# Kernel optimization log

Hardware: AMD Instinct MI355X
Metric: run time of the kernel (lower is better)

The kernel has to match this reference:

```python
import jax, jax.numpy as jnp
import numpy as np

_GELU = lambda x: jax.nn.gelu(x, approximate=False)  # torch nn.GELU default = exact erf


def setup_inputs():
    key = jax.random.key(0)
    ks = jax.random.split(key, 32)
    B, H = 16384, 768
    def p(i, shape):
        return jax.random.normal(ks[i], shape, jnp.float32) * 0.02
    return {
        "image_feat": jax.random.normal(ks[0], (B, H), jnp.float32),
        "text_feat": jax.random.normal(ks[1], (B, H), jnp.float32),
        "enhanced_image_feat": jax.random.normal(ks[2], (B, H), jnp.float32),
        "enhanced_text_feat": jax.random.normal(ks[3], (B, H), jnp.float32),
        "missing_type": jax.random.randint(ks[4], (B,), 0, 4),
        # info_encoder: H->256->64
        "info_w1": p(5, (H, 256)), "info_b1": jnp.zeros((256,), jnp.float32),
        "info_w2": p(6, (256, 64)), "info_b2": jnp.zeros((64,), jnp.float32),
        # modality_importance_predictor: H->H/2->1 (dropout inactive at eval)
        "imp_w1": p(7, (H, H // 2)), "imp_b1": jnp.zeros((H // 2,), jnp.float32),
        "imp_w2": p(8, (H // 2, 1)), "imp_b2": jnp.zeros((1,), jnp.float32),
        # feature_discriminator: H->256->64->1
        "disc_w1": p(9, (H, 256)), "disc_b1": jnp.zeros((256,), jnp.float32),
        "disc_w2": p(10, (256, 64)), "disc_b2": jnp.zeros((64,), jnp.float32),
        "disc_w3": p(11, (64, 1)), "disc_b3": jnp.zeros((1,), jnp.float32),
        # consistency_predictor: 2H->H->H/2->1
        "cons_w1": p(12, (2 * H, H)), "cons_b1": jnp.zeros((H,), jnp.float32),
        "cons_w2": p(13, (H, H // 2)), "cons_b2": jnp.zeros((H // 2,), jnp.float32),
        "cons_w3": p(14, (H // 2, 1)), "cons_b3": jnp.zeros((1,), jnp.float32),
        # task_difficulty_predictor: 2H->H->H/2->1
        "diff_w1": p(15, (2 * H, H)), "diff_b1": jnp.zeros((H,), jnp.float32),
        "diff_w2": p(16, (H, H // 2)), "diff_b2": jnp.zeros((H // 2,), jnp.float32),
        "diff_w3": p(17, (H // 2, 1)), "diff_b3": jnp.zeros((1,), jnp.float32),
    }


def _forward(image_feat, text_feat, enhanced_image_feat, enhanced_text_feat,
             info_w1, info_b1, info_w2, info_b2,
             imp_w1, imp_b1, imp_w2, imp_b2,
             disc_w1, disc_b1, disc_w2, disc_b2, disc_w3, disc_b3,
             cons_w1, cons_b1, cons_w2, cons_b2, cons_w3, cons_b3,
             diff_w1, diff_b1, diff_w2, diff_b2, diff_w3, diff_b3):
    sig = jax.nn.sigmoid

    def geometric(f):  # vectorized version of the per-sample python loop
        n = jnp.linalg.norm(f, axis=-1)
        nq = sig((n - 1.0) * 2.0)
        sp = jnp.mean((jnp.abs(f) > 0.01).astype(jnp.float32), axis=-1)
        sq = sig(jnp.std(f, axis=-1, ddof=1) * 10.0 - 1.0)  # torch.std is unbiased
        return (nq + sp + sq) / 3.0

    def information(f):
        enc = _GELU(f @ info_w1 + info_b1) @ info_w2 + info_b2  # [B,64]
        disc = jnp.round(sig(enc) * 10.0).astype(jnp.int32)     # values in 0..10
        # histogram-based entropy == the torch.unique loop (prob = count/64)
        counts = jnp.sum(disc[:, :, None] == jnp.arange(11, dtype=jnp.int32)[None, None, :], axis=1)
        prob = counts.astype(jnp.float32) / enc.shape[-1]
        ent = -jnp.sum(jnp.where(prob > 0, prob * jnp.log(prob + 1e-8), 0.0), axis=-1)
        eq = sig(ent - 2.0)
        # svd of a 1xD matrix has a single singular value = ||f||_2
        n = jnp.linalg.norm(f, axis=-1)
        cq = (n > 0.01).astype(jnp.float32) / f.shape[-1]
        fn = f / jnp.maximum(n, 1e-12)[:, None]  # F.normalize
        dq = sig(jnp.sum(fn * fn, axis=-1) - 0.5)
        return (eq + cq + dq) / 3.0

    def importance(f):
        return sig(_GELU(f @ imp_w1 + imp_b1) @ imp_w2 + imp_b2)[:, 0]

    def discrim(f):
        h = _GELU(f @ disc_w1 + disc_b1)
        h = _GELU(h @ disc_w2 + disc_b2)
        return sig(h @ disc_w3 + disc_b3)[:, 0]

    def head3(f, w1, b1, w2, b2, w3, b3):
        h = _GELU(f @ w1 + b1)
        h = _GELU(h @ w2 + b2)
        return sig(h @ w3 + b3)[:, 0]

    g_img = geometric(image_feat)
    g_txt = geometric(text_feat)
    g_eimg = geometric(enhanced_image_feat)
    g_etxt = geometric(enhanced_text_feat)
    i_img = information(image_feat)
    i_txt = information(text_feat)
    cons_o = head3(jnp.concatenate([image_feat, text_feat], -1), cons_w1, cons_b1, cons_w2, cons_b2, cons_w3, cons_b3)
    cons_e = head3(jnp.concatenate([enhanced_image_feat, enhanced_text_feat], -1), cons_w1, cons_b1, cons_w2, cons_b2, cons_w3, cons_b3)
    imp_i = importance(image_feat)
    imp_t = importance(text_feat)
    imp_ei = importance(enhanced_image_feat)
    imp_et = importance(enhanced_text_feat)
    auth_io = discrim(image_feat)
    auth_ie = discrim(enhanced_image_feat)
    auth_to = discrim(text_feat)
    auth_te = discrim(enhanced_text_feat)
    diff = head3(jnp.concatenate([enhanced_image_feat, enhanced_text_feat], -1), diff_w1, diff_b1, diff_w2, diff_b2, diff_w3, diff_b3)
    overall = (g_img + g_txt + i_img + i_txt + cons_e + (imp_i + imp_t) / 2.0) / 6.0
    return jnp.stack([g_img, g_txt, g_eimg, g_etxt, i_img, i_txt, cons_o, cons_e,
                      imp_i, imp_t, imp_ei, imp_et, auth_io, auth_ie, auth_to, auth_te,
                      diff, overall])  # [18, B]


def reference(image_feat, text_feat, enhanced_image_feat, enhanced_text_feat, missing_type,
              info_w1, info_b1, info_w2, info_b2,
              imp_w1, imp_b1, imp_w2, imp_b2,
              disc_w1, disc_b1, disc_w2, disc_b2, disc_w3, disc_b3,
              cons_w1, cons_b1, cons_w2, cons_b2, cons_w3, cons_b3,
              diff_w1, diff_b1, diff_w2, diff_b2, diff_w3, diff_b3):
    # missing_type is carried by the original forward but never used in the math
    return _forward(image_feat, text_feat, enhanced_image_feat, enhanced_text_feat,
                    info_w1, info_b1, info_w2, info_b2,
                    imp_w1, imp_b1, imp_w2, imp_b2,
                    disc_w1, disc_b1, disc_w2, disc_b2, disc_w3, disc_b3,
                    cons_w1, cons_b1, cons_w2, cons_b2, cons_w3, cons_b3,
                    diff_w1, diff_b1, diff_w2, diff_b2, diff_w3, diff_b3)
```

## Files before the change

kernel.cpp:

```cpp
#include <hip/hip_runtime.h>

typedef unsigned short bfu;
typedef __attribute__((ext_vector_type(8))) __bf16 bf16x8;
typedef __attribute__((ext_vector_type(4))) float f32x4;

__device__ __forceinline__ float bf2f(bfu u) {
    unsigned int x = ((unsigned int)u) << 16;
    return __builtin_bit_cast(float, x);
}
__device__ __forceinline__ bfu f2bf(float f) {
    unsigned int u = __builtin_bit_cast(unsigned int, f);
    unsigned int r = (u + 0x7fffu + ((u >> 16) & 1u)) >> 16;
    return (bfu)r;
}
__device__ __forceinline__ float sigm(float x) { return 1.0f / (1.0f + __expf(-x)); }
__device__ __forceinline__ float gelu_f(float x) {
    const float y = 0.7978845608f * (x + 0.044715f * x * x * x);
    const float t = 1.f - 2.f / (__expf(2.f * y) + 1.f);
    return 0.5f * x * (1.f + t);
}
__device__ __forceinline__ float gelu_x(float x) {
    return 0.5f * x * (1.0f + erff(x * 0.70710678118654752f));
}

__device__ __forceinline__ void async16(const void* g, void* l) {
    __builtin_amdgcn_global_load_lds((const __attribute__((address_space(1))) void*)g,
                                     (__attribute__((address_space(3))) void*)l, 16, 0, 0);
}

struct TDesc { const float* src; bfu* dst; int K, N, blk0; };
struct TPack { TDesc d[9]; };

__global__ __launch_bounds__(256) void transpose_k(TPack p) {
    const int bid = blockIdx.x;
    int j = 0;
#pragma unroll
    for (int i = 1; i < 9; ++i)
        if (bid >= p.d[i].blk0) j = i;
    const TDesc d = p.d[j];
    const int local = bid - d.blk0;
    const int tkn = d.K >> 6;
    const int tk = local % tkn, tn = local / tkn;
    const int k0 = tk * 64, n0 = tn * 64;
    __shared__ float tile[64][65];
    const int tx = threadIdx.x & 63, ty = threadIdx.x >> 6;
#pragma unroll
    for (int i = 0; i < 16; ++i) {
        const int r = ty * 16 + i;
        tile[r][tx] = d.src[(size_t)(k0 + r) * d.N + n0 + tx];
    }
    __syncthreads();
#pragma unroll
    for (int i = 0; i < 16; ++i) {
        const int n = ty * 16 + i;
        d.dst[(size_t)(n0 + n) * d.K + k0 + tx] = f2bf(tile[tx][n]);
    }
}

__global__ __launch_bounds__(256)
void prep_k(float* accz, int nacc, bfu* disc2pad, const float* w3,
            const float* b2, float* w3pad, float* b2pad) {
    const int i = blockIdx.x * 256 + threadIdx.x;
    if (i < nacc) accz[i] = 0.f;
    if (i < 64 * 256) disc2pad[64 * 256 + i] = 0;
    if (i < 128) {
        w3pad[i] = (i < 64) ? w3[i] : 0.f;
        b2pad[i] = (i < 64) ? b2[i] : 0.f;
    }
}

__global__ __launch_bounds__(256)
void geomcast_k(const float* F0, const float* F1, bfu* D0, bfu* D1,
                float* g0, float* g1, float* p0, float* p1) {
    const int z = blockIdx.y;
    const float* F = z ? F1 : F0;
    bfu* D = z ? D1 : D0;
    float* gout = z ? g1 : g0;
    float* part = z ? p1 : p0;
    const int wave = threadIdx.x >> 6, lane = threadIdx.x & 63;
    const int row = blockIdx.x * 4 + wave;
    const float* fr = F + (size_t)row * 768;
    bfu* dr = D + (size_t)row * 768;
    float sum = 0.f, ss = 0.f, cnt = 0.f;
#pragma unroll
    for (int i = 0; i < 3; ++i) {
        const float4 v = *(const float4*)(fr + i * 256 + lane * 4);
        sum += v.x + v.y + v.z + v.w;
        ss += v.x * v.x + v.y * v.y + v.z * v.z + v.w * v.w;
        cnt += ((fabsf(v.x) > 0.01f) ? 1.f : 0.f) + ((fabsf(v.y) > 0.01f) ? 1.f : 0.f) +
               ((fabsf(v.z) > 0.01f) ? 1.f : 0.f) + ((fabsf(v.w) > 0.01f) ? 1.f : 0.f);
        ushort4 b;
        b.x = f2bf(v.x); b.y = f2bf(v.y); b.z = f2bf(v.z); b.w = f2bf(v.w);
        *(ushort4*)(dr + i * 256 + lane * 4) = b;
    }
#pragma unroll
    for (int off = 32; off; off >>= 1) {
        sum += __shfl_xor(sum, off);
        ss  += __shfl_xor(ss, off);
        cnt += __shfl_xor(cnt, off);
    }
    if (lane == 0) {
        const float n = sqrtf(ss);
        const float nq = sigm((n - 1.f) * 2.f);
        const float sp = cnt * (1.f / 768.f);
        float var = (ss - sum * sum * (1.f / 768.f)) * (1.f / 767.f);
        var = fmaxf(var, 0.f);
        const float sq = sigm(sqrtf(var) * 10.f - 1.f);
        gout[row] = (nq + sp + sq) * (1.f / 3.f);
        if (part) {
            const float cq = (n > 0.01f) ? (1.f / 768.f) : 0.f;
            const float nc = fmaxf(n, 1e-12f);
            const float dq = sigm(ss / (nc * nc) - 0.5f);
            part[row] = (cq + dq) * (1.f / 3.f);
        }
    }
}

struct Half {
    const bfu* W;
    const float* bias;
    const float* dotw;
    bfu* C;
    float* acc;
    int ldc, mode;
};
struct Seg {
    const bfu* A; const bfu* A2;
    Half h[2];
    int K, Ksplit, lda, Mtiles;
};
struct SegPack { Seg s[7]; };

__global__ __launch_bounds__(512, 2)
void gemm_k(SegPack p) {
    constexpr int BK = 64;
    __shared__ bfu LDS[65536];
    bfu* As0 = LDS;
    bfu* As1 = LDS + 16384;
    bfu* Ws0 = LDS + 32768;
    bfu* Ws1 = LDS + 49152;

    const int NTt = gridDim.x;
    const int g = blockIdx.y * NTt + blockIdx.x;
    const int G8 = NTt * 8;
    const int m = (g / G8) * 8 + (g & 7);
    const int n = (g % G8) >> 3;
    const Seg sg = p.s[n];
    if (m >= sg.Mtiles) return;
    const int t = threadIdx.x;
    const int wave = t >> 6, lane = t & 63;
    const int row_l = lane & 15, kq = lane >> 4;
    const int m0 = m * 256;
    const int wm = wave >> 2;
    const int wn = wave & 3;
    const int half = wn >> 1;

    const int r0 = t >> 3;
    const int cc = ((t & 7) ^ (r0 & 7)) << 3;
    const bfu* pA[4];
    const bfu* pW[4];
#pragma unroll
    for (int i = 0; i < 4; ++i)
        pA[i] = sg.A + (size_t)(m0 + r0 + 64 * i) * sg.lda + cc;
#pragma unroll
    for (int i = 0; i < 2; ++i) {
        pW[i]     = sg.h[0].W + (size_t)(r0 + 64 * i) * sg.K + cc;
        pW[2 + i] = sg.h[1].W + (size_t)(r0 + 64 * i) * sg.K + cc;
    }
    const int nkt = sg.K >> 6;
    const int ktsw = (sg.Ksplit < sg.K) ? (sg.Ksplit >> 6) : 0x7fffffff;

    f32x4 acc[8][4] = {};

    auto stageA = [&](int sn, bfu* Ad) {
        if (sn == ktsw) {
#pragma unroll
            for (int i = 0; i < 4; ++i)
                pA[i] = sg.A2 + (size_t)(m0 + r0 + 64 * i) * sg.lda + cc;
        }
#pragma unroll
        for (int i = 0; i < 4; ++i)
            async16(pA[i], Ad + ((i * 512 + wave * 64) << 3));
#pragma unroll
        for (int i = 0; i < 4; ++i) pA[i] += BK;
    };
    auto ldF = [&](const bfu* base, int row, int ks) -> bf16x8 {
        return *(const bf16x8*)(base + row * BK + (((ks * 4 + kq) ^ (row & 7)) << 3));
    };

#pragma unroll
    for (int i = 0; i < 4; ++i)
        async16(pW[i], Ws0 + ((i * 512 + wave * 64) << 3));
#pragma unroll
    for (int i = 0; i < 4; ++i) pW[i] += BK;
    stageA(0, As0);
#pragma unroll
    for (int i = 0; i < 4; ++i)
        async16(pW[i], Ws1 + ((i * 512 + wave * 64) << 3));
#pragma unroll
    for (int i = 0; i < 4; ++i) pW[i] += BK;
    asm volatile("s_waitcnt vmcnt(4)" ::: "memory");
    __builtin_amdgcn_s_barrier();

    auto do_iter = [&](bfu* Acur, bfu* Aoth, bfu* Wcur, int kt) {
        bf16x8 af[4], b0[4], b1[4];
#pragma unroll
        for (int q = 0; q < 4; ++q)
            af[q] = ldF(Acur, wm * 128 + q * 16 + row_l, 0);
#pragma unroll
        for (int ni = 0; ni < 4; ++ni) {
            const int rB = wn * 64 + ni * 16 + row_l;
            b0[ni] = ldF(Wcur, rB, 0);
            b1[ni] = ldF(Wcur, rB, 1);
        }
        if (kt + 1 < nkt) stageA(kt + 1, Aoth);
        __builtin_amdgcn_s_barrier();
        asm volatile("s_waitcnt lgkmcnt(0)" ::: "memory");
        __builtin_amdgcn_sched_barrier(0);
        __builtin_amdgcn_s_setprio(1);
#pragma unroll
        for (int q = 0; q < 4; ++q)
#pragma unroll
            for (int ni = 0; ni < 4; ++ni)
                acc[q][ni] = __builtin_amdgcn_mfma_f32_16x16x32_bf16(af[q], b0[ni], acc[q][ni], 0, 0, 0);
        __builtin_amdgcn_s_setprio(0);
        __builtin_amdgcn_s_barrier();
#pragma unroll
        for (int q = 0; q < 4; ++q)
            af[q] = ldF(Acur, wm * 128 + q * 16 + row_l, 1);
        if (kt + 2 < nkt) {
            async16(pW[0], Wcur + ((0 * 512 + wave * 64) << 3));
            async16(pW[1], Wcur + ((1 * 512 + wave * 64) << 3));
        }
        __builtin_amdgcn_s_barrier();
        asm volatile("s_waitcnt lgkmcnt(0)" ::: "memory");
        __builtin_amdgcn_sched_barrier(0);
        __builtin_amdgcn_s_setprio(1);
#pragma unroll
        for (int q = 0; q < 4; ++q)
#pragma unroll
            for (int ni = 0; ni < 4; ++ni)
                acc[q][ni] = __builtin_amdgcn_mfma_f32_16x16x32_bf16(af[q], b1[ni], acc[q][ni], 0, 0, 0);
        __builtin_amdgcn_s_setprio(0);
        __builtin_amdgcn_s_barrier();
#pragma unroll
        for (int q = 0; q < 4; ++q)
            af[q] = ldF(Acur, wm * 128 + 64 + q * 16 + row_l, 0);
        if (kt + 2 < nkt) {
            async16(pW[2], Wcur + ((2 * 512 + wave * 64) << 3));
            async16(pW[3], Wcur + ((3 * 512 + wave * 64) << 3));
#pragma unroll
            for (int i = 0; i < 4; ++i) pW[i] += BK;
        }
        __builtin_amdgcn_s_barrier();
        asm volatile("s_waitcnt lgkmcnt(0)" ::: "memory");
        __builtin_amdgcn_sched_barrier(0);
        __builtin_amdgcn_s_setprio(1);
#pragma unroll
        for (int q = 0; q < 4; ++q)
#pragma unroll
            for (int ni = 0; ni < 4; ++ni)
                acc[4 + q][ni] = __builtin_amdgcn_mfma_f32_16x16x32_bf16(af[q], b0[ni], acc[4 + q][ni], 0, 0, 0);
        __builtin_amdgcn_s_setprio(0);
        __builtin_amdgcn_s_barrier();
#pragma unroll
        for (int q = 0; q < 4; ++q)
            af[q] = ldF(Acur, wm * 128 + 64 + q * 16 + row_l, 1);
        if (kt + 2 < nkt) { asm volatile("s_waitcnt vmcnt(4)" ::: "memory"); }
        else              { asm volatile("s_waitcnt vmcnt(0)" ::: "memory"); }
        __builtin_amdgcn_s_barrier();
        asm volatile("s_waitcnt lgkmcnt(0)" ::: "memory");
        __builtin_amdgcn_sched_barrier(0);
        __builtin_amdgcn_s_setprio(1);
#pragma unroll
        for (int q = 0; q < 4; ++q)
#pragma unroll
            for (int ni = 0; ni < 4; ++ni)
                acc[4 + q][ni] = __builtin_amdgcn_mfma_f32_16x16x32_bf16(af[q], b1[ni], acc[4 + q][ni], 0, 0, 0);
        __builtin_amdgcn_s_setprio(0);
        __builtin_amdgcn_s_barrier();
    };

    for (int kt = 0; kt < nkt; kt += 2) {
        do_iter(As0, As1, Ws0, kt);
        do_iter(As1, As0, Ws1, kt + 1);
    }

    const Half hh = sg.h[half];
    if (hh.mode == 0) {
#pragma unroll
        for (int ni = 0; ni < 4; ++ni) {
            const int lcol = (wn & 1) * 64 + ni * 16 + row_l;
            const float bv = hh.bias[lcol];
#pragma unroll
            for (int mi = 0; mi < 8; ++mi)
#pragma unroll
                for (int r = 0; r < 4; ++r) {
                    const int row = m0 + wm * 128 + mi * 16 + kq * 4 + r;
                    hh.C[(size_t)row * hh.ldc + lcol] = f2bf(gelu_f(acc[mi][ni][r] + bv));
                }
        }
    } else if (hh.mode == 2) {
#pragma unroll
        for (int ni = 0; ni < 4; ++ni) {
            const int lcol = (wn & 1) * 64 + ni * 16 + row_l;
            const float bv = hh.bias[lcol];
#pragma unroll
            for (int mi = 0; mi < 8; ++mi)
#pragma unroll
                for (int r = 0; r < 4; ++r) {
                    const int row = m0 + wm * 128 + mi * 16 + kq * 4 + r;
                    hh.C[(size_t)row * hh.ldc + lcol] = f2bf(gelu_x(acc[mi][ni][r] + bv));
                }
        }
    } else if (hh.mode == 1) {
#pragma unroll
        for (int mi = 0; mi < 8; ++mi)
#pragma unroll
            for (int r = 0; r < 4; ++r) {
                float s = 0.f;
#pragma unroll
                for (int ni = 0; ni < 4; ++ni) {
                    const int lcol = (wn & 1) * 64 + ni * 16 + row_l;
                    s += hh.dotw[lcol] * gelu_f(acc[mi][ni][r] + hh.bias[lcol]);
                }
                s += __shfl_xor(s, 1); s += __shfl_xor(s, 2);
                s += __shfl_xor(s, 4); s += __shfl_xor(s, 8);
                if (row_l == 0)
                    atomicAdd(hh.acc + m0 + wm * 128 + mi * 16 + kq * 4 + r, s);
            }
    }
}

__global__ __launch_bounds__(256)
void gemm64ent_k(const bfu* __restrict__ A, const bfu* __restrict__ W,
                 const float* __restrict__ bias, const float* __restrict__ part,
                 float* out, int B, int K, int lda) {
    constexpr int BK = 64, MT = 2, NT = 4;
    __shared__ __align__(16) float smemf[12288];
    bfu* As0 = (bfu*)smemf;
    bfu* Ws0 = (bfu*)smemf + 128 * BK;
    bfu* As1 = (bfu*)smemf + 192 * BK;
    bfu* Ws1 = (bfu*)smemf + 320 * BK;
    float* ET = smemf;
    const int t = threadIdx.x;
    const int wave = t >> 6, lane = t & 63;
    const int row_l = lane & 15, kq = lane >> 4;
    const int m0 = blockIdx.x * 128;
    const int wrow0 = wave * 32;
    f32x4 acc[MT][NT] = {};
    const int nkt = K / BK;

    const int r0 = t >> 3;
    const int cc = ((t & 7) ^ (r0 & 7)) << 3;
    const size_t strA = (size_t)32 * lda;
    const size_t strW = (size_t)32 * K;
    const bfu* pA[4];
    const bfu* pW[2];
#pragma unroll
    for (int i = 0; i < 4; ++i)
        pA[i] = A + (size_t)(m0 + r0) * lda + cc + i * strA;
#pragma unroll
    for (int i = 0; i < 2; ++i)
        pW[i] = W + (size_t)r0 * K + cc + i * strW;

    auto stage = [&](bfu* Ad, bfu* Wd) {
#pragma unroll
        for (int i = 0; i < 4; ++i)
            async16(pA[i], Ad + ((i * 256 + wave * 64) << 3));
#pragma unroll
        for (int i = 0; i < 2; ++i)
            async16(pW[i], Wd + ((i * 256 + wave * 64) << 3));
#pragma unroll
        for (int i = 0; i < 4; ++i) pA[i] += BK;
#pragma unroll
        for (int i = 0; i < 2; ++i) pW[i] += BK;
    };
    auto compute = [&](const bfu* Ab, const bfu* Wb) {
#pragma unroll
        for (int ks = 0; ks < 2; ++ks) {
            bf16x8 af[MT], bfr[NT];
#pragma unroll
            for (int mi = 0; mi < MT; ++mi) {
                const int rA = wrow0 + mi * 16 + row_l;
                af[mi] = *(const bf16x8*)(Ab + rA * BK + (((ks * 4 + kq) ^ (rA & 7)) << 3));
            }
#pragma unroll
            for (int ni = 0; ni < NT; ++ni) {
                const int rB = ni * 16 + row_l;
                bfr[ni] = *(const bf16x8*)(Wb + rB * BK + (((ks * 4 + kq) ^ (rB & 7)) << 3));
            }
#pragma unroll
            for (int mi = 0; mi < MT; ++mi)
#pragma unroll
                for (int ni = 0; ni < NT; ++ni)
                    acc[mi][ni] = __builtin_amdgcn_mfma_f32_16x16x32_bf16(af[mi], bfr[ni], acc[mi][ni], 0, 0, 0);
        }
    };

    stage(As0, Ws0);
    __syncthreads();
    for (int kt = 0; kt < nkt; kt += 2) {
        stage(As1, Ws1);
        compute(As0, Ws0);
        __syncthreads();
        if (kt + 2 < nkt) stage(As0, Ws0);
        compute(As1, Ws1);
        __syncthreads();
    }

#pragma unroll
    for (int mi = 0; mi < MT; ++mi)
#pragma unroll
        for (int ni = 0; ni < NT; ++ni) {
            const int col = ni * 16 + row_l;
            const float bv = bias[col];
#pragma unroll
            for (int r = 0; r < 4; ++r)
                ET[(wrow0 + mi * 16 + kq * 4 + r) * 65 + col] = acc[mi][ni][r] + bv;
        }
    __syncthreads();
    if (t < 128) {
        int cnt[11];
#pragma unroll
        for (int b = 0; b < 11; ++b) cnt[b] = 0;
        for (int j = 0; j < 64; ++j) {
            const int d = (int)rintf(sigm(ET[t * 65 + j]) * 10.f);
#pragma unroll
            for (int b = 0; b < 11; ++b) cnt[b] += (d == b);
        }
        float ent = 0.f;
#pragma unroll
        for (int b = 0; b < 11; ++b) {
            if (cnt[b] > 0) {
                const float pp = (float)cnt[b] * (1.f / 64.f);
                ent -= pp * __logf(pp + 1e-8f);
            }
        }
        const int row = m0 + t;
        const int orow = (row < B) ? 4 : 5;
        const int rl = (row < B) ? row : row - B;
        out[(size_t)orow * B + rl] = part[row] + sigm(ent - 2.f) * (1.f / 3.f);
    }
}

__global__ __launch_bounds__(256)
void finalize_k(float* out, const float* a_imp1, const float* a_imp2,
                const float* a_co, const float* a_ce, const float* a_df,
                const float* a_d1, const float* a_d2,
                const float* imp_b2, const float* disc_b3,
                const float* cons_b3, const float* diff_b3, int B) {
    const int i = blockIdx.x * 256 + threadIdx.x;
    if (i >= B) return;
    const float ib = imp_b2[0], db = disc_b3[0], cb = cons_b3[0], fb = diff_b3[0];
    const float o6 = sigm(a_co[i] + cb);
    const float o7 = sigm(a_ce[i] + cb);
    const float o8 = sigm(a_imp1[i] + ib);
    const float o9 = sigm(a_imp1[B + i] + ib);
    out[6 * B + i] = o6;
    out[7 * B + i] = o7;
    out[8 * B + i] = o8;
    out[9 * B + i] = o9;
    out[10 * B + i] = sigm(a_imp2[i] + ib);
    out[11 * B + i] = sigm(a_imp2[B + i] + ib);
    out[12 * B + i] = sigm(a_d1[i] + db);
    out[14 * B + i] = sigm(a_d1[B + i] + db);
    out[13 * B + i] = sigm(a_d2[i] + db);
    out[15 * B + i] = sigm(a_d2[B + i] + db);
    out[16 * B + i] = sigm(a_df[i] + fb);
    const float v = out[0 * B + i] + out[1 * B + i] + out[4 * B + i] + out[5 * B + i] +
                    o7 + 0.5f * (o8 + o9);
    out[17 * B + i] = v * (1.f / 6.f);
}

extern "C" void kernel_launch(void* const* d_in, const int* in_sizes, int n_in,
                              void* d_out, int out_size, void* d_ws, size_t ws_size,
                              hipStream_t stream) {
    const int B = in_sizes[4];
    const int B2 = 2 * B;
    float* out = (float*)d_out;
    const float* img  = (const float*)d_in[0];
    const float* txt  = (const float*)d_in[1];
    const float* eimg = (const float*)d_in[2];
    const float* etxt = (const float*)d_in[3];
    const float* info_w1 = (const float*)d_in[5];  const float* info_b1 = (const float*)d_in[6];
    const float* info_w2 = (const float*)d_in[7];  const float* info_b2 = (const float*)d_in[8];
    const float* imp_w1  = (const float*)d_in[9];  const float* imp_b1  = (const float*)d_in[10];
    const float* imp_w2  = (const float*)d_in[11]; const float* imp_b2  = (const float*)d_in[12];
    const float* disc_w1 = (const float*)d_in[13]; const float* disc_b1 = (const float*)d_in[14];
    const float* disc_w2 = (const float*)d_in[15]; const float* disc_b2 = (const float*)d_in[16];
    const float* disc_w3 = (const float*)d_in[17]; const float* disc_b3 = (const float*)d_in[18];
    const float* cons_w1 = (const float*)d_in[19]; const float* cons_b1 = (const float*)d_in[20];
    const float* cons_w2 = (const float*)d_in[21]; const float* cons_b2 = (const float*)d_in[22];
    const float* cons_w3 = (const float*)d_in[23]; const float* cons_b3 = (const float*)d_in[24];
    const float* diff_w1 = (const float*)d_in[25]; const float* diff_b1 = (const float*)d_in[26];
    const float* diff_w2 = (const float*)d_in[27]; const float* diff_b2 = (const float*)d_in[28];
    const float* diff_w3 = (const float*)d_in[29]; const float* diff_b3 = (const float*)d_in[30];

    char* wsp = (char*)d_ws;
    size_t off = 0;
    auto alloc = [&](size_t bytes) -> void* {
        void* p = wsp + off;
        off += (bytes + 255) & ~(size_t)255;
        return p;
    };
    bfu* info1t = (bfu*)alloc((size_t)256 * 768 * 2);
    bfu* info2t = (bfu*)alloc((size_t)64 * 256 * 2);
    bfu* imp1t  = (bfu*)alloc((size_t)384 * 768 * 2);
    bfu* disc1t = (bfu*)alloc((size_t)256 * 768 * 2);
    bfu* disc2p = (bfu*)alloc((size_t)128 * 256 * 2);
    bfu* cons1t = (bfu*)alloc((size_t)768 * 1536 * 2);
    bfu* cons2t = (bfu*)alloc((size_t)384 * 768 * 2);
    bfu* diff1t = (bfu*)alloc((size_t)768 * 1536 * 2);
    bfu* diff2t = (bfu*)alloc((size_t)384 * 768 * 2);
    float* w3pad = (float*)alloc(128 * 4);
    float* b2pad = (float*)alloc(128 * 4);
    float* part = (float*)alloc((size_t)B2 * 4);
    float* accz = (float*)alloc((size_t)11 * B * 4);
    float* a_imp1 = accz;
    float* a_imp2 = accz + B2;
    float* a_co = accz + 2 * B2;
    float* a_ce = a_co + B;
    float* a_df = a_ce + B;
    float* a_d1 = a_df + B;
    float* a_d2 = a_d1 + B2;
    bfu* fA01 = (bfu*)alloc((size_t)B2 * 768 * 2);
    bfu* X    = (bfu*)alloc((size_t)B * 2048 * 2);
    bfu* Hd   = X;
    bfu* Hi   = X + (size_t)B * 512;
    bfu* Hc_c = X + (size_t)B * 512;
    bfu* Hc_d = X + (size_t)B * 1280;
    (void)ws_size; (void)n_in; (void)out_size;

    prep_k<<<dim3((11 * B + 255) / 256), 256, 0, stream>>>(accz, 11 * B, disc2p,
                                                           disc_w3, disc_b2, w3pad, b2pad);
    TPack tp;
    int blk = 0, ti = 0;
    auto setd = [&](const float* s, bfu* d, int K, int N) {
        tp.d[ti++] = {s, d, K, N, blk};
        blk += (K / 64) * (N / 64);
    };
    setd(info_w1, info1t, 768, 256);
    setd(info_w2, info2t, 256, 64);
    setd(imp_w1, imp1t, 768, 384);
    setd(disc_w1, disc1t, 768, 256);
    setd(disc_w2, disc2p, 256, 64);
    setd(cons_w1, cons1t, 1536, 768);
    setd(cons_w2, cons2t, 768, 384);
    setd(diff_w1, diff1t, 1536, 768);
    setd(diff_w2, diff2t, 768, 384);
    transpose_k<<<dim3(blk), 256, 0, stream>>>(tp);

    auto h_st = [&](const bfu* W, const float* b, bfu* C, int ldc, int mode) -> Half {
        return Half{W, b, nullptr, C, nullptr, ldc, mode};
    };
    auto h_dt = [&](const bfu* W, const float* b, const float* dw, float* acc) -> Half {
        return Half{W, b, dw, nullptr, acc, 0, 1};
    };
    auto h_skip = [&](const bfu* W) -> Half {
        return Half{W, nullptr, nullptr, nullptr, nullptr, 0, 3};
    };
    auto seg = [&](const bfu* A, const bfu* A2, Half h0, Half h1,
                   int K, int Ksplit, int lda, int Mt) -> Seg {
        return Seg{A, A2, {h0, h1}, K, Ksplit, lda, Mt};
    };
    const bfu* fB = fA01 + (size_t)B * 768;
    const int MT2 = B2 / 256, MT1 = B / 256;

    geomcast_k<<<dim3(B / 4, 2), 256, 0, stream>>>(img, txt, fA01, (bfu*)fB,
                                                   out + 0 * B, out + 1 * B, part, part + B);
    {
        SegPack p;
        p.s[0] = seg(fA01, nullptr,
                     h_st(info1t, info_b1, Hi, 256, 2),
                     h_st(info1t + (size_t)128 * 768, info_b1 + 128, Hi + 128, 256, 2),
                     768, 768, 768, MT2);
        p.s[1] = seg(fA01, nullptr,
                     h_st(disc1t, disc_b1, Hd, 256, 0),
                     h_st(disc1t + (size_t)128 * 768, disc_b1 + 128, Hd + 128, 256, 0),
                     768, 768, 768, MT2);
        p.s[2] = seg(fA01, nullptr,
                     h_dt(imp1t, imp_b1, imp_w2, a_imp1),
                     h_dt(imp1t + (size_t)128 * 768, imp_b1 + 128, imp_w2 + 128, a_imp1),
                     768, 768, 768, MT2);
        p.s[3] = seg(fA01, nullptr,
                     h_dt(imp1t + (size_t)256 * 768, imp_b1 + 256, imp_w2 + 256, a_imp1),
                     h_skip(imp1t),
                     768, 768, 768, MT2);
        gemm_k<<<dim3(4, MT2), 512, 0, stream>>>(p);
    }
    gemm64ent_k<<<dim3(B2 / 128), 256, 0, stream>>>(Hi, info2t, info_b2, part, out, B, 256, 256);
    {
        SegPack p;
        for (int i = 0; i < 3; ++i)
            p.s[i] = seg(fA01, fB,
                         h_st(cons1t + (size_t)256 * i * 1536, cons_b1 + 256 * i,
                              Hc_c + 256 * i, 768, 0),
                         h_st(cons1t + (size_t)(256 * i + 128) * 1536, cons_b1 + 256 * i + 128,
                              Hc_c + 256 * i + 128, 768, 0),
                         1536, 768, 768, MT1);
        p.s[3] = seg(Hd, nullptr,
                     h_dt(disc2p, b2pad, w3pad, a_d1),
                     h_skip(disc2p),
                     256, 256, 256, MT2);
        gemm_k<<<dim3(4, MT2), 512, 0, stream>>>(p);
    }

    geomcast_k<<<dim3(B / 4, 2), 256, 0, stream>>>(eimg, etxt, fA01, (bfu*)fB,
                                                   out + 2 * B, out + 3 * B, nullptr, nullptr);
    {
        SegPack p;
        p.s[0] = seg(fA01, nullptr,
                     h_dt(imp1t, imp_b1, imp_w2, a_imp2),
                     h_dt(imp1t + (size_t)128 * 768, imp_b1 + 128, imp_w2 + 128, a_imp2),
                     768, 768, 768, MT2);
        p.s[1] = seg(fA01, nullptr,
                     h_st(disc1t, disc_b1, Hd, 256, 0),
                     h_st(disc1t + (size_t)128 * 768, disc_b1 + 128, Hd + 128, 256, 0),
                     768, 768, 768, MT2);
        p.s[2] = seg(fA01, nullptr,
                     h_dt(imp1t + (size_t)256 * 768, imp_b1 + 256, imp_w2 + 256, a_imp2),
                     h_skip(imp1t),
                     768, 768, 768, MT2);
        p.s[3] = seg(Hc_c, nullptr,
                     h_dt(cons2t, cons_b2, cons_w3, a_co),
                     h_dt(cons2t + (size_t)128 * 768, cons_b2 + 128, cons_w3 + 128, a_co),
                     768, 768, 768, MT1);
        p.s[4] = seg(Hc_c, nullptr,
                     h_dt(cons2t + (size_t)256 * 768, cons_b2 + 256, cons_w3 + 256, a_co),
                     h_skip(cons2t),
                     768, 768, 768, MT1);
        gemm_k<<<dim3(5, MT2), 512, 0, stream>>>(p);
    }
    {
        SegPack p;
        for (int i = 0; i < 6; ++i)
            p.s[i] = seg(fA01, fB,
                         h_st(cons1t + (size_t)128 * i * 1536, cons_b1 + 128 * i,
                              Hc_c + 128 * i, 768, 0),
                         h_st(diff1t + (size_t)128 * i * 1536, diff_b1 + 128 * i,
                              Hc_d + 128 * i, 768, 0),
                         1536, 768, 768, MT1);
        p.s[6] = seg(Hd, nullptr,
                     h_dt(disc2p, b2pad, w3pad, a_d2),
                     h_skip(disc2p),
                     256, 256, 256, MT2);
        gemm_k<<<dim3(7, MT2), 512, 0, stream>>>(p);
    }
    {
        SegPack p;
        p.s[0] = seg(Hc_c, nullptr,
                     h_dt(cons2t, cons_b2, cons_w3, a_ce),
                     h_dt(cons2t + (size_t)128 * 768, cons_b2 + 128, cons_w3 + 128, a_ce),
                     768, 768, 768, MT1);
        p.s[1] = seg(Hc_c, nullptr,
                     h_dt(cons2t + (size_t)256 * 768, cons_b2 + 256, cons_w3 + 256, a_ce),
                     h_skip(cons2t),
                     768, 768, 768, MT1);
        p.s[2] = seg(Hc_d, nullptr,
                     h_dt(diff2t, diff_b2, diff_w3, a_df),
                     h_dt(diff2t + (size_t)128 * 768, diff_b2 + 128, diff_w3 + 128, a_df),
                     768, 768, 768, MT1);
        p.s[3] = seg(Hc_d, nullptr,
                     h_dt(diff2t + (size_t)256 * 768, diff_b2 + 256, diff_w3 + 256, a_df),
                     h_skip(diff2t),
                     768, 768, 768, MT1);
        gemm_k<<<dim3(4, MT1), 512, 0, stream>>>(p);
    }

    finalize_k<<<dim3((B + 255) / 256), 256, 0, stream>>>(out, a_imp1, a_imp2, a_co, a_ce,
                                                          a_df, a_d1, a_d2,
                                                          imp_b2, disc_b3, cons_b3, diff_b3, B);
}
```

Before: 788.9 us.

## Replace hand-scheduled ping-pong GEMM loop with simple double-buffered pipeline

Drops the finely interleaved schedule that split each K tile into four phases, each with its own barrier, setprio and waitcnt. It is replaced by a plain double-buffered loop that stages the next A and W tiles, computes the full current tile, then calls __syncthreads. This lets the compiler schedule LDS reads and MFMAs freely and cuts the number of barriers per tile. The risks are losing the explicit overlap of global loads with MFMA and relying on __syncthreads' implicit vmcnt wait. It also stages tile kt+1 before checking that it exists, which assumes the number of K tiles is even.

```diff
diff --git a/kernel.cpp b/kernel.cpp
--- a/kernel.cpp
+++ b/kernel.cpp
@@ -184,106 +184,48 @@
 #pragma unroll
         for (int i = 0; i < 4; ++i) pA[i] += BK;
     };
+    auto stageW = [&](bfu* Wd) {
+#pragma unroll
+        for (int i = 0; i < 4; ++i)
+            async16(pW[i], Wd + ((i * 512 + wave * 64) << 3));
+#pragma unroll
+        for (int i = 0; i < 4; ++i) pW[i] += BK;
+    };
     auto ldF = [&](const bfu* base, int row, int ks) -> bf16x8 {
         return *(const bf16x8*)(base + row * BK + (((ks * 4 + kq) ^ (row & 7)) << 3));
     };
-
-#pragma unroll
-    for (int i = 0; i < 4; ++i)
-        async16(pW[i], Ws0 + ((i * 512 + wave * 64) << 3));
-#pragma unroll
-    for (int i = 0; i < 4; ++i) pW[i] += BK;
-    stageA(0, As0);
-#pragma unroll
-    for (int i = 0; i < 4; ++i)
-        async16(pW[i], Ws1 + ((i * 512 + wave * 64) << 3));
-#pragma unroll
-    for (int i = 0; i < 4; ++i) pW[i] += BK;
-    asm volatile("s_waitcnt vmcnt(4)" ::: "memory");
-    __builtin_amdgcn_s_barrier();
-
-    auto do_iter = [&](bfu* Acur, bfu* Aoth, bfu* Wcur, int kt) {
-        bf16x8 af[4], b0[4], b1[4];
-#pragma unroll
-        for (int q = 0; q < 4; ++q)
-            af[q] = ldF(Acur, wm * 128 + q * 16 + row_l, 0);
+    auto compute = [&](const bfu* Ab, const bfu* Wb) {
+        bf16x8 b0[4], b1[4];
 #pragma unroll
         for (int ni = 0; ni < 4; ++ni) {
             const int rB = wn * 64 + ni * 16 + row_l;
-            b0[ni] = ldF(Wcur, rB, 0);
-            b1[ni] = ldF(Wcur, rB, 1);
-        }
-        if (kt + 1 < nkt) stageA(kt + 1, Aoth);
-        __builtin_amdgcn_s_barrier();
-        asm volatile("s_waitcnt lgkmcnt(0)" ::: "memory");
-        __builtin_amdgcn_sched_barrier(0);
-        __builtin_amdgcn_s_setprio(1);
-#pragma unroll
-        for (int q = 0; q < 4; ++q)
+            b0[ni] = ldF(Wb, rB, 0);
+            b1[ni] = ldF(Wb, rB, 1);
+        }
+#pragma unroll
+        for (int mi = 0; mi < 8; ++mi) {
+            const int rA = wm * 128 + mi * 16 + row_l;
+            const bf16x8 a0 = ldF(Ab, rA, 0);
+            const bf16x8 a1 = ldF(Ab, rA, 1);
 #pragma unroll
             for (int ni = 0; ni < 4; ++ni)
-                acc[q][ni] = __builtin_amdgcn_mfma_f32_16x16x32_bf16(af[q], b0[ni], acc[q][ni], 0, 0, 0);
-        __builtin_amdgcn_s_setprio(0);
-        __builtin_amdgcn_s_barrier();
-#pragma unroll
-        for (int q = 0; q < 4; ++q)
-            af[q] = ldF(Acur, wm * 128 + q * 16 + row_l, 1);
-        if (kt + 2 < nkt) {
-            async16(pW[0], Wcur + ((0 * 512 + wave * 64) << 3));
-            async16(pW[1], Wcur + ((1 * 512 + wave * 64) << 3));
-        }
-        __builtin_amdgcn_s_barrier();
-        asm volatile("s_waitcnt lgkmcnt(0)" ::: "memory");
-        __builtin_amdgcn_sched_barrier(0);
-        __builtin_amdgcn_s_setprio(1);
-#pragma unroll
-        for (int q = 0; q < 4; ++q)
+                acc[mi][ni] = __builtin_amdgcn_mfma_f32_16x16x32_bf16(a0, b0[ni], acc[mi][ni], 0, 0, 0);
 #pragma unroll
             for (int ni = 0; ni < 4; ++ni)
-                acc[q][ni] = __builtin_amdgcn_mfma_f32_16x16x32_bf16(af[q], b1[ni], acc[q][ni], 0, 0, 0);
-        __builtin_amdgcn_s_setprio(0);
-        __builtin_amdgcn_s_barrier();
-#pragma unroll
-        for (int q = 0; q < 4; ++q)
-            af[q] = ldF(Acur, wm * 128 + 64 + q * 16 + row_l, 0);
-        if (kt + 2 < nkt) {
-            async16(pW[2], Wcur + ((2 * 512 + wave * 64) << 3));
-            async16(pW[3], Wcur + ((3 * 512 + wave * 64) << 3));
-#pragma unroll
-            for (int i = 0; i < 4; ++i) pW[i] += BK;
-        }
-        __builtin_amdgcn_s_barrier();
-        asm volatile("s_waitcnt lgkmcnt(0)" ::: "memory");
-        __builtin_amdgcn_sched_barrier(0);
-        __builtin_amdgcn_s_setprio(1);
-#pragma unroll
-        for (int q = 0; q < 4; ++q)
-#pragma unroll
-            for (int ni = 0; ni < 4; ++ni)
-                acc[4 + q][ni] = __builtin_amdgcn_mfma_f32_16x16x32_bf16(af[q], b0[ni], acc[4 + q][ni], 0, 0, 0);
-        __builtin_amdgcn_s_setprio(0);
-        __builtin_amdgcn_s_barrier();
-#pragma unroll
-        for (int q = 0; q < 4; ++q)
-            af[q] = ldF(Acur, wm * 128 + 64 + q * 16 + row_l, 1);
-        if (kt + 2 < nkt) { asm volatile("s_waitcnt vmcnt(4)" ::: "memory"); }
-        else              { asm volatile("s_waitcnt vmcnt(0)" ::: "memory"); }
-        __builtin_amdgcn_s_barrier();
-        asm volatile("s_waitcnt lgkmcnt(0)" ::: "memory");
-        __builtin_amdgcn_sched_barrier(0);
-        __builtin_amdgcn_s_setprio(1);
-#pragma unroll
-        for (int q = 0; q < 4; ++q)
-#pragma unroll
-            for (int ni = 0; ni < 4; ++ni)
-                acc[4 + q][ni] = __builtin_amdgcn_mfma_f32_16x16x32_bf16(af[q], b1[ni], acc[4 + q][ni], 0, 0, 0);
-        __builtin_amdgcn_s_setprio(0);
-        __builtin_amdgcn_s_barrier();
-    };
-
+                acc[mi][ni] = __builtin_amdgcn_mfma_f32_16x16x32_bf16(a1, b1[ni], acc[mi][ni], 0, 0, 0);
+        }
+    };
+
+    stageA(0, As0);
+    stageW(Ws0);
+    __syncthreads();
     for (int kt = 0; kt < nkt; kt += 2) {
-        do_iter(As0, As1, Ws0, kt);
-        do_iter(As1, As0, Ws1, kt + 1);
+        stageA(kt + 1, As1); stageW(Ws1);
+        compute(As0, Ws0);
+        __syncthreads();
+        if (kt + 2 < nkt) { stageA(kt + 2, As0); stageW(Ws0); }
+        compute(As1, Ws1);
+        __syncthreads();
     }
 
     const Half hh = sg.h[half];
```

Result: faster. 768.7 us (-2.6%).
